# Kernel optimization log

Hardware: AMD Instinct MI355X
Metric: run time of the kernel (lower is better)

## Reference

```python
import jax, jax.numpy as jnp
import numpy as np

B, T, D, H = 256, 128, 256, 512


def setup_inputs() -> dict:
    key = jax.random.key(0)
    ks = jax.random.split(key, 21)
    n = jax.random.normal
    u = jax.random.uniform
    return {
        "x": n(ks[0], (B, T, D), jnp.float32),
        "dt": u(ks[1], (B, T, D), jnp.float32),
        "mask": jnp.round(u(ks[2], (B, T, D), jnp.float32)),  # binary observed-mask
        "tp": u(ks[3], (B, T, 1), jnp.float32),
        "x_mean": n(ks[4], (D,), jnp.float32),
        "h0": n(ks[5], (1, H), jnp.float32),
        "c0": n(ks[6], (1, H), jnp.float32),
        "w_gx": n(ks[7], (D, D), jnp.float32) * 0.1,
        "h_gx": n(ks[8], (D,), jnp.float32) * 0.1,
        "w_gh": n(ks[9], (D, H), jnp.float32) * 0.1,
        "h_gh": n(ks[10], (H,), jnp.float32) * 0.1,
        "w_t": n(ks[11], (1, H), jnp.float32),
        "h_t": n(ks[12], (H,), jnp.float32),
        "W_ih": n(ks[13], (4 * H, D), jnp.float32) * 0.05,
        "W_hh": n(ks[14], (4 * H, H), jnp.float32) * 0.05,
        "b_ih": n(ks[15], (4 * H,), jnp.float32) * 0.05,
        "b_hh": n(ks[16], (4 * H,), jnp.float32) * 0.05,
        "out_W1": n(ks[17], (H, 10), jnp.float32) * 0.1,
        "out_b1": n(ks[18], (10,), jnp.float32) * 0.1,
        "out_W2": n(ks[19], (10, 2), jnp.float32),
        "out_b2": n(ks[20], (2,), jnp.float32),
    }


def reference(x, dt, mask, tp, x_mean, h0, c0, w_gx, h_gx, w_gh, h_gh,
              w_t, h_t, W_ih, W_hh, b_ih, b_hh, out_W1, out_b1, out_W2, out_b2):
    Bn, Tn, _ = x.shape
    h = jnp.broadcast_to(h0, (Bn, h0.shape[1]))
    c = jnp.broadcast_to(c0, (Bn, c0.shape[1]))
    x_prev0 = jnp.zeros_like(x[:, 0, :])  # unused at step 0 (is_first masks it out)
    is_first = jnp.concatenate([jnp.ones((1,), x.dtype), jnp.zeros((Tn - 1,), x.dtype)])

    def step(carry, inps):
        h, c, x_prev = carry
        x_t, dt_t, m_t, tp_t, first = inps
        # decay gates (GRU-D style)
        gamma_x = jnp.exp(-jnp.maximum(0.0, dt_t @ w_gx + h_gx))  # [B,D]
        gamma_h = jnp.exp(-jnp.maximum(0.0, dt_t @ w_gh + h_gh))  # [B,H]
        h = gamma_h * h
        c = gamma_h * c
        # imputation: at t==0 use x_mean, else decayed previous raw x toward mean
        imput = jnp.where(first > 0, x_mean, gamma_x * x_prev + (1.0 - gamma_x) * x_mean)
        xs = x_t * m_t + (1.0 - m_t) * imput
        # time gate from tp
        gt = jax.nn.sigmoid(tp_t @ w_t + h_t)  # [B,H]
        # LSTMCell (torch gate order: i, f, g, o)
        gates = xs @ W_ih.T + b_ih + h @ W_hh.T + b_hh  # [B,4H]
        i_g, f_g, g_g, o_g = jnp.split(gates, 4, axis=1)
        c1 = jax.nn.sigmoid(f_g) * c + jax.nn.sigmoid(i_g) * jnp.tanh(g_g)
        h1 = jax.nn.sigmoid(o_g) * jnp.tanh(c1)
        h1 = gt * h1
        c1 = gt * c1
        # output head: Linear->sigmoid->Linear->sigmoid->softmax
        z = jax.nn.sigmoid(h1 @ out_W1 + out_b1)
        z = jax.nn.sigmoid(z @ out_W2 + out_b2)
        out = jax.nn.softmax(z, axis=1)
        return (h1, c1, x_t), (out, xs)

    seq = (jnp.swapaxes(x, 0, 1), jnp.swapaxes(dt, 0, 1),
           jnp.swapaxes(mask, 0, 1), jnp.swapaxes(tp, 0, 1), is_first)
    _, (outs, xhats) = jax.lax.scan(step, (h, c, x_prev0), seq)
    return outs, xhats  # [T,B,2], [T,B,D]
```

## Files before the change

### kernel.cpp

```cpp
#include <hip/hip_runtime.h>
#include <hip/hip_bf16.h>
#include <math.h>

namespace {

constexpr int Bn = 256;
constexpr int Tn = 128;
constexpr int Dn = 256;
constexpr int Hn = 512;
constexpr int BT = Bn * Tn;

constexpr int AP = 776;
constexpr int GP = 264;
constexpr int GS = 68;
constexpr unsigned KC = 2654435769u;

typedef short bf8_t __attribute__((ext_vector_type(8)));
typedef float f32x4 __attribute__((ext_vector_type(4)));
typedef unsigned int u32x4 __attribute__((ext_vector_type(4)));

__device__ __forceinline__ float sigm(float v) { return 1.0f / (1.0f + expf(-v)); }

__device__ __forceinline__ unsigned short f2bf(float f) {
  union { __hip_bfloat16 h; unsigned short u; } v;
  v.h = __float2bfloat16(f);
  return v.u;
}
__device__ __forceinline__ float bf2f(unsigned short u) {
  union { unsigned int i; float f; } v;
  v.i = ((unsigned int)u) << 16;
  return v.f;
}

__global__ void k_nonce(unsigned* __restrict__ np) {
  if (threadIdx.x == 0 && blockIdx.x == 0) np[0] = np[0] + 1u;
}

__global__ __launch_bounds__(256) void k_cvt_dt(const float* __restrict__ src,
                                                unsigned short* __restrict__ dst) {
  size_t i = (size_t)blockIdx.x * 256 + threadIdx.x;
  float4 v = ((const float4*)src)[i];
  uint2 o;
  o.x = (unsigned)f2bf(v.x) | ((unsigned)f2bf(v.y) << 16);
  o.y = (unsigned)f2bf(v.z) | ((unsigned)f2bf(v.w) << 16);
  ((uint2*)dst)[i] = o;
}

__global__ __launch_bounds__(256) void k_cvt_wgh(const float* __restrict__ w,
                                                 unsigned short* __restrict__ wT) {
  int o = blockIdx.x * 256 + threadIdx.x;
  int n = o >> 8, k = o & 255;
  wT[o] = f2bf(w[(size_t)k * Hn + n]);
}

__global__ __launch_bounds__(256) void k_gamma_mfma(
    const unsigned short* __restrict__ dtb,
    const unsigned short* __restrict__ wT,
    const float* __restrict__ bias,
    float* __restrict__ outg) {
  __shared__ unsigned short Abf[128 * GP];
  __shared__ unsigned short Bbf[64 * GP];
  int tid = threadIdx.x;
  int n0 = blockIdx.x * 64;
  int bb = blockIdx.y;
  const u32x4* asrc = (const u32x4*)(dtb + (size_t)bb * 128 * Dn);
#pragma unroll
  for (int i = 0; i < 16; ++i) {
    int c = tid + 256 * i;
    *(u32x4*)(&Abf[(size_t)(c >> 5) * GP + (c & 31) * 8]) = asrc[c];
  }
  const u32x4* bsrc = (const u32x4*)(wT + (size_t)n0 * Dn);
#pragma unroll
  for (int i = 0; i < 8; ++i) {
    int c = tid + 256 * i;
    *(u32x4*)(&Bbf[(size_t)(c >> 5) * GP + (c & 31) * 8]) = bsrc[c];
  }
  int lane = tid & 63, w = tid >> 6;
  int ln = lane & 15, qd = lane >> 4;
  float bn[4];
#pragma unroll
  for (int j = 0; j < 4; ++j) bn[j] = bias[n0 + 16 * j + ln];
  __syncthreads();
  f32x4 acc[2][4] = {};
  const unsigned short* a0 = &Abf[(size_t)(32 * w + ln) * GP + qd * 8];
  const unsigned short* a1 = &Abf[(size_t)(32 * w + 16 + ln) * GP + qd * 8];
#pragma unroll
  for (int ks = 0; ks < 8; ++ks) {
    bf8_t af0 = *(const bf8_t*)(a0 + ks * 32);
    bf8_t af1 = *(const bf8_t*)(a1 + ks * 32);
#pragma unroll
    for (int j = 0; j < 4; ++j) {
      bf8_t bf = *(const bf8_t*)(&Bbf[(size_t)(16 * j + ln) * GP + qd * 8 + ks * 32]);
      acc[0][j] = __builtin_amdgcn_mfma_f32_16x16x32_bf16(af0, bf, acc[0][j], 0, 0, 0);
      acc[1][j] = __builtin_amdgcn_mfma_f32_16x16x32_bf16(af1, bf, acc[1][j], 0, 0, 0);
    }
  }
#pragma unroll
  for (int mt = 0; mt < 2; ++mt)
#pragma unroll
    for (int r = 0; r < 4; ++r) {
      int t = 32 * w + 16 * mt + qd * 4 + r;
#pragma unroll
      for (int j = 0; j < 4; ++j) {
        float v = acc[mt][j][r] + bn[j];
        outg[((size_t)t * Bn + bb) * Hn + n0 + 16 * j + ln] = expf(-fmaxf(v, 0.f));
      }
    }
}

__global__ __launch_bounds__(256) void k_xs(const float* __restrict__ dt,
                                            const float* __restrict__ w,
                                            const float* __restrict__ bias,
                                            const float* __restrict__ x,
                                            const float* __restrict__ mask,
                                            const float* __restrict__ xmean,
                                            float* __restrict__ out_xs,
                                            unsigned short* __restrict__ out_bf) {
  __shared__ float As[64][17];
  __shared__ float Bs[16][64];
  int tid = threadIdx.x;
  int tx = tid & 15, ty = tid >> 4;
  int m0 = blockIdx.y * 64, n0 = blockIdx.x * 64;
  float acc[4][4] = {};
  for (int k0 = 0; k0 < Dn; k0 += 16) {
    {
      int ml = tid >> 2, kk = (tid & 3) * 4;
      float4 v = *(const float4*)(dt + (size_t)(m0 + ml) * Dn + k0 + kk);
      As[ml][kk + 0] = v.x; As[ml][kk + 1] = v.y;
      As[ml][kk + 2] = v.z; As[ml][kk + 3] = v.w;
    }
    {
      int kb = (tid >> 6) * 4, nl = tid & 63;
#pragma unroll
      for (int r = 0; r < 4; ++r)
        Bs[kb + r][nl] = w[(size_t)(k0 + kb + r) * Dn + n0 + nl];
    }
    __syncthreads();
#pragma unroll
    for (int kk = 0; kk < 16; ++kk) {
      float a[4], b[4];
#pragma unroll
      for (int i = 0; i < 4; ++i) a[i] = As[ty + 16 * i][kk];
#pragma unroll
      for (int j = 0; j < 4; ++j) b[j] = Bs[kk][tx + 16 * j];
#pragma unroll
      for (int i = 0; i < 4; ++i)
#pragma unroll
        for (int j = 0; j < 4; ++j) acc[i][j] += a[i] * b[j];
    }
    __syncthreads();
  }
#pragma unroll
  for (int j = 0; j < 4; ++j) {
    int d = n0 + tx + 16 * j;
    float bv = bias[d];
    float xm = xmean[d];
#pragma unroll
    for (int i = 0; i < 4; ++i) {
      int m = m0 + ty + 16 * i;
      int b = m >> 7, tt = m & (Tn - 1);
      float g = expf(-fmaxf(acc[i][j] + bv, 0.0f));
      float imput = (tt == 0) ? xm
                              : g * x[(size_t)(m - 1) * Dn + d] + (1.0f - g) * xm;
      float xv = x[(size_t)m * Dn + d];
      float mv = mask[(size_t)m * Dn + d];
      float xsv = xv * mv + (1.0f - mv) * imput;
      size_t oi = ((size_t)tt * Bn + b) * Dn + d;
      out_xs[oi] = xsv;
      out_bf[oi] = f2bf(xsv);
    }
  }
}

__global__ __launch_bounds__(256) void k_init(const float* __restrict__ h0,
                                              const float* __restrict__ gammaT,
                                              unsigned int* __restrict__ hdec,
                                              const unsigned* __restrict__ np) {
  int i = blockIdx.x * 256 + threadIdx.x;
  unsigned nb = np[0] << 8;
  unsigned key0 = nb * KC;
  unsigned key1 = (nb + 1u) * KC;
  int h = (i & 255) * 2;
  int b = i >> 8;
  float g0 = gammaT[(size_t)b * Hn + h];
  float g1 = gammaT[(size_t)b * Hn + h + 1];
  unsigned pay = (unsigned)f2bf(h0[h] * g0) | ((unsigned)f2bf(h0[h + 1] * g1) << 16);
  uint2* buf0 = (uint2*)hdec;
  uint2* buf1 = buf0 + (size_t)Bn * 256;
  uint2 v0; v0.x = pay; v0.y = pay ^ key0;
  uint2 v1; v1.x = 0u;  v1.y = key1 ^ 1u;
  buf0[i] = v0;
  buf1[i] = v1;
}

__global__ __launch_bounds__(256, 1) void k_scan(
    const unsigned short* __restrict__ xs_bf,
    const float* __restrict__ gammaT,
    unsigned int* __restrict__ hdec_tag,
    unsigned short* __restrict__ h_bf,
    const float* __restrict__ c0,
    const float* __restrict__ W_ih,
    const float* __restrict__ W_hh,
    const float* __restrict__ b_ih, const float* __restrict__ b_hh,
    const float* __restrict__ tp,
    const float* __restrict__ w_t, const float* __restrict__ h_t,
    const unsigned* __restrict__ np) {
  __shared__ unsigned short Wlds[64 * AP];
  __shared__ unsigned short Alds[32 * AP];
  __shared__ float Gs[32 * GS];
  int tid = threadIdx.x;
  int bt = blockIdx.x & 7;
  int ht = blockIdx.x >> 3;
  int b0 = bt * 32, h0b = ht * 16;
  unsigned nb = np[0] << 8;

  for (int idx = tid; idx < 64 * 192; idx += 256) {
    int c = idx / 192;
    int s = idx - c * 192;
    int kg = s * 4;
    int g = c >> 4, hu = c & 15;
    int jw = g * Hn + h0b + hu;
    float4 wv;
    if (kg < Dn) wv = *(const float4*)(W_ih + (size_t)jw * Dn + kg);
    else         wv = *(const float4*)(W_hh + (size_t)jw * Hn + (kg - Dn));
    unsigned int u01 = (unsigned int)f2bf(wv.x) | ((unsigned int)f2bf(wv.y) << 16);
    unsigned int u23 = (unsigned int)f2bf(wv.z) | ((unsigned int)f2bf(wv.w) << 16);
    *(unsigned int*)(&Wlds[(size_t)c * AP + kg]) = u01;
    *(unsigned int*)(&Wlds[(size_t)c * AP + kg + 2]) = u23;
  }

  int bl = tid >> 3;
  int hp = tid & 7;
  int hloc = 2 * hp;
  int b = b0 + bl;
  float bias[4][2];
#pragma unroll
  for (int g = 0; g < 4; ++g)
#pragma unroll
    for (int u = 0; u < 2; ++u) {
      int jw = g * Hn + h0b + hloc + u;
      bias[g][u] = b_ih[jw] + b_hh[jw];
    }
  float wtv[2], htv[2], creg[2];
#pragma unroll
  for (int u = 0; u < 2; ++u) {
    wtv[u] = w_t[h0b + hloc + u];
    htv[u] = h_t[h0b + hloc + u];
    creg[u] = c0[h0b + hloc + u];
  }

  int lane = tid & 63, wv4 = tid >> 6;
  int ln = lane & 15, qd = lane >> 4;
  int mrow = 16 * (wv4 & 1) + ln;
  int ncol = 32 * (wv4 >> 1);
  const unsigned short* abase = &Alds[(size_t)mrow * AP + qd * 8];
  const unsigned short* bb0 = &Wlds[(size_t)(ncol + ln) * AP + qd * 8];
  const unsigned short* bb1 = &Wlds[(size_t)(ncol + 16 + ln) * AP + qd * 8];
  unsigned int* pstore =
      hdec_tag + ((size_t)b * 256 + 8 * (size_t)ht + hp) * 2;
  __syncthreads();

  for (int t = 0; t < Tn; ++t) {
    unsigned key = (nb + (unsigned)t) * KC;
    float2 gam0 = *(const float2*)(gammaT + ((size_t)t * Bn + b) * Hn + h0b + hloc);
    float2 gam1 = (t + 1 < Tn)
        ? *(const float2*)(gammaT + ((size_t)(t + 1) * Bn + b) * Hn + h0b + hloc)
        : make_float2(0.f, 0.f);
    float tpv = tp[(size_t)b * Tn + t];

    {
      const float4* xsrc = (const float4*)(xs_bf + ((size_t)t * Bn + b0) * Dn);
#pragma unroll
      for (int i = 0; i < 4; ++i) {
        int c = tid + 256 * i;
        *(float4*)(&Alds[(size_t)(c >> 5) * AP + (c & 31) * 8]) = xsrc[c];
      }
    }

    {
      const unsigned int* hsrc =
          hdec_tag + (size_t)(t & 1) * (Bn * 256 * 2) + (size_t)b0 * 256 * 2;
      u32x4 hv[16];
      int ok = 0, spins = 0;
      while (!ok) {
#pragma unroll
        for (int i = 0; i < 16; ++i) {
          int q = tid + 256 * i;
          const void* p = hsrc + (size_t)q * 4;
          asm volatile("global_load_dwordx4 %0, %1, off sc0 sc1"
                       : "=&v"(hv[i]) : "v"(p) : "memory");
        }
        asm volatile("s_waitcnt vmcnt(0)" ::: "memory");
        ok = 1;
#pragma unroll
        for (int i = 0; i < 16; ++i)
          ok &= (hv[i][1] == (hv[i][0] ^ key)) & (hv[i][3] == (hv[i][2] ^ key));
        if (!ok) {
          if (++spins > 300000) break;
          __builtin_amdgcn_s_sleep(1);
        }
      }
#pragma unroll
      for (int i = 0; i < 16; ++i) {
        int q = tid + 256 * i;
        int blr = q >> 7;
        int p0 = (q & 127) * 2;
        uint2 pv; pv.x = hv[i][0]; pv.y = hv[i][2];
        *(uint2*)(&Alds[(size_t)blr * AP + 256 + 2 * p0]) = pv;
      }
    }
    __syncthreads();

    f32x4 acc0 = {0.f, 0.f, 0.f, 0.f};
    f32x4 acc1 = {0.f, 0.f, 0.f, 0.f};
#pragma unroll
    for (int ks = 0; ks < 24; ++ks) {
      bf8_t a = *(const bf8_t*)(abase + ks * 32);
      bf8_t b0f = *(const bf8_t*)(bb0 + ks * 32);
      bf8_t b1f = *(const bf8_t*)(bb1 + ks * 32);
      acc0 = __builtin_amdgcn_mfma_f32_16x16x32_bf16(a, b0f, acc0, 0, 0, 0);
      acc1 = __builtin_amdgcn_mfma_f32_16x16x32_bf16(a, b1f, acc1, 0, 0, 0);
    }

#pragma unroll
    for (int r = 0; r < 4; ++r) {
      int grow = 16 * (wv4 & 1) + qd * 4 + r;
      Gs[grow * GS + ncol + ln] = acc0[r];
      Gs[grow * GS + ncol + 16 + ln] = acc1[r];
    }
    __syncthreads();

    {
      float2 ip = *(const float2*)(&Gs[bl * GS + hloc]);
      float2 fp = *(const float2*)(&Gs[bl * GS + 16 + hloc]);
      float2 gp = *(const float2*)(&Gs[bl * GS + 32 + hloc]);
      float2 op = *(const float2*)(&Gs[bl * GS + 48 + hloc]);
      float h1[2], hd[2];
      float gam0a[2] = {gam0.x, gam0.y}, gam1a[2] = {gam1.x, gam1.y};
      float ipa[2] = {ip.x, ip.y}, fpa[2] = {fp.x, fp.y};
      float gpa[2] = {gp.x, gp.y}, opa[2] = {op.x, op.y};
#pragma unroll
      for (int u = 0; u < 2; ++u) {
        float c1 = sigm(fpa[u] + bias[1][u]) * (creg[u] * gam0a[u]) +
                   sigm(ipa[u] + bias[0][u]) * tanhf(gpa[u] + bias[2][u]);
        float gtv = sigm(tpv * wtv[u] + htv[u]);
        h1[u] = gtv * sigm(opa[u] + bias[3][u]) * tanhf(c1);
        creg[u] = gtv * c1;
        hd[u] = h1[u] * gam1a[u];
      }
      if (t + 1 < Tn) {
        unsigned keyn = (nb + (unsigned)(t + 1)) * KC;
        unsigned dpk =
            (unsigned)f2bf(hd[0]) | ((unsigned)f2bf(hd[1]) << 16);
        unsigned long long val =
            (unsigned long long)dpk | ((unsigned long long)(dpk ^ keyn) << 32);
        const void* dp = pstore + (size_t)((t + 1) & 1) * (Bn * 256 * 2);
        asm volatile("global_store_dwordx2 %0, %1, off sc0 sc1"
                     :: "v"(dp), "v"(val) : "memory");
      }
      unsigned hpk =
          (unsigned)f2bf(h1[0]) | ((unsigned)f2bf(h1[1]) << 16);
      *(unsigned int*)(h_bf + ((size_t)t * Bn + b) * Hn + h0b + hloc) = hpk;
    }
  }
}

__global__ __launch_bounds__(256) void k_head(const unsigned short* __restrict__ h_bf,
                                              const float* __restrict__ W1,
                                              const float* __restrict__ b1,
                                              const float* __restrict__ W2,
                                              const float* __restrict__ b2,
                                              float* __restrict__ outs) {
  __shared__ float sW1[Hn * 10];
  for (int i = threadIdx.x; i < Hn * 10; i += 256) sW1[i] = W1[i];
  __syncthreads();
  int idx = blockIdx.x * 256 + threadIdx.x;
  const uint4* row = (const uint4*)(h_bf + (size_t)idx * Hn);
  float z1[10];
#pragma unroll
  for (int k = 0; k < 10; ++k) z1[k] = b1[k];
  for (int hq = 0; hq < Hn / 8; ++hq) {
    uint4 u = row[hq];
    float hv[8];
    hv[0] = bf2f(u.x & 0xffff); hv[1] = bf2f(u.x >> 16);
    hv[2] = bf2f(u.y & 0xffff); hv[3] = bf2f(u.y >> 16);
    hv[4] = bf2f(u.z & 0xffff); hv[5] = bf2f(u.z >> 16);
    hv[6] = bf2f(u.w & 0xffff); hv[7] = bf2f(u.w >> 16);
    int hb = hq * 8;
#pragma unroll
    for (int c = 0; c < 8; ++c)
#pragma unroll
      for (int k = 0; k < 10; ++k) z1[k] += hv[c] * sW1[(hb + c) * 10 + k];
  }
#pragma unroll
  for (int k = 0; k < 10; ++k) z1[k] = sigm(z1[k]);
  float z2[2];
#pragma unroll
  for (int c = 0; c < 2; ++c) {
    float v = b2[c];
#pragma unroll
    for (int k = 0; k < 10; ++k) v += z1[k] * W2[k * 2 + c];
    z2[c] = sigm(v);
  }
  float mx = fmaxf(z2[0], z2[1]);
  float e0 = expf(z2[0] - mx), e1 = expf(z2[1] - mx);
  float s = e0 + e1;
  outs[(size_t)idx * 2 + 0] = e0 / s;
  outs[(size_t)idx * 2 + 1] = e1 / s;
}

}

extern "C" void kernel_launch(void* const* d_in, const int* in_sizes, int n_in,
                              void* d_out, int out_size, void* d_ws,
                              size_t ws_size, hipStream_t stream) {
  (void)in_sizes; (void)n_in; (void)out_size; (void)ws_size;
  const float* x     = (const float*)d_in[0];
  const float* dt    = (const float*)d_in[1];
  const float* mask  = (const float*)d_in[2];
  const float* tp    = (const float*)d_in[3];
  const float* xmean = (const float*)d_in[4];
  const float* h0    = (const float*)d_in[5];
  const float* c0    = (const float*)d_in[6];
  const float* w_gx  = (const float*)d_in[7];
  const float* h_gx  = (const float*)d_in[8];
  const float* w_gh  = (const float*)d_in[9];
  const float* h_gh  = (const float*)d_in[10];
  const float* w_t   = (const float*)d_in[11];
  const float* h_t   = (const float*)d_in[12];
  const float* W_ih  = (const float*)d_in[13];
  const float* W_hh  = (const float*)d_in[14];
  const float* b_ih  = (const float*)d_in[15];
  const float* b_hh  = (const float*)d_in[16];
  const float* oW1   = (const float*)d_in[17];
  const float* ob1   = (const float*)d_in[18];
  const float* oW2   = (const float*)d_in[19];
  const float* ob2   = (const float*)d_in[20];

  float* out  = (float*)d_out;
  float* outs = out;
  float* xhat = out + (size_t)Tn * Bn * 2;

  float* ws = (float*)d_ws;
  float* gammaT = ws;
  unsigned short* xs_bf  = (unsigned short*)(gammaT + (size_t)BT * Hn);
  unsigned short* h_bf   = xs_bf + (size_t)BT * Dn;
  unsigned int* hdec_tag = (unsigned int*)(h_bf + (size_t)BT * Hn);
  unsigned short* dt_bf  = (unsigned short*)(hdec_tag + 2 * (size_t)Bn * 256 * 2);
  unsigned short* wghT   = dt_bf + (size_t)BT * Dn;
  unsigned* np = (unsigned*)(wghT + (size_t)Hn * Dn);

  k_nonce<<<1, 64, 0, stream>>>(np);
  k_cvt_dt<<<BT * Dn / 4 / 256, 256, 0, stream>>>(dt, dt_bf);
  k_cvt_wgh<<<Hn * Dn / 256, 256, 0, stream>>>(w_gh, wghT);
  k_gamma_mfma<<<dim3(Hn / 64, Bn), 256, 0, stream>>>(dt_bf, wghT, h_gh, gammaT);
  k_xs<<<dim3(Dn / 64, BT / 64), 256, 0, stream>>>(dt, w_gx, h_gx, x, mask,
                                                   xmean, xhat, xs_bf);
  k_init<<<(Bn * 256) / 256, 256, 0, stream>>>(h0, gammaT, hdec_tag, np);
  k_scan<<<256, 256, 0, stream>>>(xs_bf, gammaT, hdec_tag, h_bf, c0, W_ih, W_hh,
                                  b_ih, b_hh, tp, w_t, h_t, np);
  k_head<<<BT / 256, 256, 0, stream>>>(h_bf, oW1, ob1, oW2, ob2, outs);
}
```

Measured before the change: 822.2 us.

## Overlap recurrent h loads with x-part MFMAs and prefetch next-step inputs

Each timestep now issues the polled global loads for the decayed hidden state first, then runs the x-input third of the MFMA reduction (k-steps 0–7) while those loads are in flight. The h tile is written to LDS only after that, followed by the remaining h-part k-steps. The next step's xs tile is prefetched into registers at the end of each iteration, and gamma for step t+1 is carried over instead of reloaded. `__syncthreads` is replaced by explicit lgkmcnt waits, raw barriers and sched_barriers. This hides part of the cross-block handoff latency on the serial recurrence, at the cost of more registers and more delicate ordering.

After: 893.6 us. 1.09x slower.

```diff
diff --git a/kernel.cpp b/kernel.cpp
--- a/kernel.cpp
+++ b/kernel.cpp
@@ -258,31 +258,68 @@
   const unsigned short* bb1 = &Wlds[(size_t)(ncol + 16 + ln) * AP + qd * 8];
   unsigned int* pstore =
       hdec_tag + ((size_t)b * 256 + 8 * (size_t)ht + hp) * 2;
+
+  float4 xr[4];
+  {
+    const float4* xsrc = (const float4*)(xs_bf + (size_t)0 * Bn * Dn + (size_t)b0 * Dn);
+#pragma unroll
+    for (int i = 0; i < 4; ++i) xr[i] = xsrc[tid + 256 * i];
+  }
+  float2 gamc = *(const float2*)(gammaT + (size_t)b * Hn + h0b + hloc);
   __syncthreads();
 
   for (int t = 0; t < Tn; ++t) {
     unsigned key = (nb + (unsigned)t) * KC;
-    float2 gam0 = *(const float2*)(gammaT + ((size_t)t * Bn + b) * Hn + h0b + hloc);
+
+#pragma unroll
+    for (int i = 0; i < 4; ++i) {
+      int c = tid + 256 * i;
+      *(float4*)(&Alds[(size_t)(c >> 5) * AP + (c & 31) * 8]) = xr[i];
+    }
+
+    const unsigned int* hsrc =
+        hdec_tag + (size_t)(t & 1) * (Bn * 256 * 2) + (size_t)b0 * 256 * 2;
+    u32x4 hv[16];
+#pragma unroll
+    for (int i = 0; i < 16; ++i) {
+      int q = tid + 256 * i;
+      const void* p = hsrc + (size_t)q * 4;
+      asm volatile("global_load_dwordx4 %0, %1, off sc0 sc1"
+                   : "=&v"(hv[i]) : "v"(p) : "memory");
+    }
+
+    float2 gam0 = gamc;
     float2 gam1 = (t + 1 < Tn)
         ? *(const float2*)(gammaT + ((size_t)(t + 1) * Bn + b) * Hn + h0b + hloc)
         : make_float2(0.f, 0.f);
     float tpv = tp[(size_t)b * Tn + t];
 
+    asm volatile("s_waitcnt lgkmcnt(0)" ::: "memory");
+    __builtin_amdgcn_s_barrier();
+    __builtin_amdgcn_sched_barrier(0);
+
+    f32x4 acc0 = {0.f, 0.f, 0.f, 0.f};
+    f32x4 acc1 = {0.f, 0.f, 0.f, 0.f};
+#pragma unroll
+    for (int ks = 0; ks < 8; ++ks) {
+      bf8_t a = *(const bf8_t*)(abase + ks * 32);
+      bf8_t b0f = *(const bf8_t*)(bb0 + ks * 32);
+      bf8_t b1f = *(const bf8_t*)(bb1 + ks * 32);
+      acc0 = __builtin_amdgcn_mfma_f32_16x16x32_bf16(a, b0f, acc0, 0, 0, 0);
+      acc1 = __builtin_amdgcn_mfma_f32_16x16x32_bf16(a, b1f, acc1, 0, 0, 0);
+    }
+
     {
-      const float4* xsrc = (const float4*)(xs_bf + ((size_t)t * Bn + b0) * Dn);
-#pragma unroll
-      for (int i = 0; i < 4; ++i) {
-        int c = tid + 256 * i;
-        *(float4*)(&Alds[(size_t)(c >> 5) * AP + (c & 31) * 8]) = xsrc[c];
-      }
-    }
-
-    {
-      const unsigned int* hsrc =
-          hdec_tag + (size_t)(t & 1) * (Bn * 256 * 2) + (size_t)b0 * 256 * 2;
-      u32x4 hv[16];
-      int ok = 0, spins = 0;
+      asm volatile("s_waitcnt vmcnt(0)" ::: "memory");
+      __builtin_amdgcn_sched_barrier(0);
+      int ok = 1;
+#pragma unroll
+      for (int i = 0; i < 16; ++i)
+        ok &= (hv[i][1] == (hv[i][0] ^ key)) & (hv[i][3] == (hv[i][2] ^ key));
+      int spins = 0;
       while (!ok) {
+        if (++spins > 300000) break;
+        __builtin_amdgcn_s_sleep(1);
 #pragma unroll
         for (int i = 0; i < 16; ++i) {
           int q = tid + 256 * i;
@@ -291,30 +328,29 @@
                        : "=&v"(hv[i]) : "v"(p) : "memory");
         }
         asm volatile("s_waitcnt vmcnt(0)" ::: "memory");
+        __builtin_amdgcn_sched_barrier(0);
         ok = 1;
 #pragma unroll
         for (int i = 0; i < 16; ++i)
           ok &= (hv[i][1] == (hv[i][0] ^ key)) & (hv[i][3] == (hv[i][2] ^ key));
-        if (!ok) {
-          if (++spins > 300000) break;
-          __builtin_amdgcn_s_sleep(1);
-        }
       }
-#pragma unroll
-      for (int i = 0; i < 16; ++i) {
-        int q = tid + 256 * i;
-        int blr = q >> 7;
-        int p0 = (q & 127) * 2;
-        uint2 pv; pv.x = hv[i][0]; pv.y = hv[i][2];
-        *(uint2*)(&Alds[(size_t)blr * AP + 256 + 2 * p0]) = pv;
-      }
-    }
-    __syncthreads();
-
-    f32x4 acc0 = {0.f, 0.f, 0.f, 0.f};
-    f32x4 acc1 = {0.f, 0.f, 0.f, 0.f};
-#pragma unroll
-    for (int ks = 0; ks < 24; ++ks) {
+    }
+
+#pragma unroll
+    for (int i = 0; i < 16; ++i) {
+      int q = tid + 256 * i;
+      int blr = q >> 7;
+      int p0 = (q & 127) * 2;
+      uint2 pv; pv.x = hv[i][0]; pv.y = hv[i][2];
+      *(uint2*)(&Alds[(size_t)blr * AP + 256 + 2 * p0]) = pv;
+    }
+
+    asm volatile("s_waitcnt lgkmcnt(0)" ::: "memory");
+    __builtin_amdgcn_s_barrier();
+    __builtin_amdgcn_sched_barrier(0);
+
+#pragma unroll
+    for (int ks = 8; ks < 24; ++ks) {
       bf8_t a = *(const bf8_t*)(abase + ks * 32);
       bf8_t b0f = *(const bf8_t*)(bb0 + ks * 32);
       bf8_t b1f = *(const bf8_t*)(bb1 + ks * 32);
@@ -328,7 +364,10 @@
       Gs[grow * GS + ncol + ln] = acc0[r];
       Gs[grow * GS + ncol + 16 + ln] = acc1[r];
     }
-    __syncthreads();
+
+    asm volatile("s_waitcnt lgkmcnt(0)" ::: "memory");
+    __builtin_amdgcn_s_barrier();
+    __builtin_amdgcn_sched_barrier(0);
 
     {
       float2 ip = *(const float2*)(&Gs[bl * GS + hloc]);
@@ -362,6 +401,14 @@
           (unsigned)f2bf(h1[0]) | ((unsigned)f2bf(h1[1]) << 16);
       *(unsigned int*)(h_bf + ((size_t)t * Bn + b) * Hn + h0b + hloc) = hpk;
     }
+
+    if (t + 1 < Tn) {
+      const float4* xsrc =
+          (const float4*)(xs_bf + ((size_t)(t + 1) * Bn + b0) * Dn);
+#pragma unroll
+      for (int i = 0; i < 4; ++i) xr[i] = xsrc[tid + 256 * i];
+    }
+    gamc = gam1;
   }
 }
 
```
